# Optimization experiments

Hardware: AMD Instinct MI355X
Metric: run time of the kernel (lower is better)

## Reference

```python
import jax, jax.numpy as jnp
import numpy as np
import math

EMBED_DIM = 1024
NUM_HEADS = 16
HEAD_DIM = EMBED_DIM // NUM_HEADS
B, S = 4, 2048


def setup_inputs() -> dict:
    key = jax.random.key(0)
    ks = jax.random.split(key, 9)
    scale = 1.0 / math.sqrt(EMBED_DIM)
    def lin(k):
        kw, kb = jax.random.split(k)
        W = jax.random.uniform(kw, (EMBED_DIM, EMBED_DIM), jnp.float32, -scale, scale)
        b = jax.random.uniform(kb, (EMBED_DIM,), jnp.float32, -scale, scale)
        return W, b
    Wq, bq = lin(ks[0]); Wk, bk = lin(ks[1]); Wv, bv = lin(ks[2]); Wo, bo = lin(ks[3])
    x = jax.random.normal(ks[4], (B, S, EMBED_DIM), jnp.float32)
    return {"x": x, "Wq": Wq, "bq": bq, "Wk": Wk, "bk": bk,
            "Wv": Wv, "bv": bv, "Wo": Wo, "bo": bo}


def reference(x, Wq, bq, Wk, bk, Wv, bv, Wo, bo):
    Bx, Sx, E = x.shape
    def proj(W, b):
        y = jnp.einsum('bse,oe->bso', x, W) + b
        return y.reshape(Bx, Sx, NUM_HEADS, HEAD_DIM).transpose(0, 2, 1, 3)  # [B,H,S,D]
    q = proj(Wq, bq)
    k = proj(Wk, bk)
    v = proj(Wv, bv)
    scores = jnp.einsum('bhsd,bhtd->bhst', q, k) / math.sqrt(HEAD_DIM)
    # causal mask (paged_cache is None, seq_len > 1)
    causal = jnp.tril(jnp.ones((Sx, Sx), dtype=bool))
    scores = jnp.where(causal[None, None], scores, -jnp.inf)
    attn = jax.nn.softmax(scores, axis=-1)
    out = jnp.einsum('bhst,bhtd->bhsd', attn, v)
    out = out.transpose(0, 2, 1, 3).reshape(Bx, Sx, E)
    return jnp.einsum('bse,oe->bso', out, Wo) + bo
```

## Files before the change

### kernel.cpp

```cpp
#include <hip/hip_runtime.h>
#include <hip/hip_bf16.h>
#include <stdint.h>

#define EDIM 1024
#define NH   16
#define HD   64
#define BB   4
#define SS   2048
#define MROWS (BB*SS)

typedef __bf16 bf16x8 __attribute__((ext_vector_type(8)));
typedef __bf16 bf16x4 __attribute__((ext_vector_type(4)));
typedef float  f32x4  __attribute__((ext_vector_type(4)));
typedef float  f32x16 __attribute__((ext_vector_type(16)));
typedef int    int2v  __attribute__((ext_vector_type(2)));

__device__ __forceinline__ void async16(const void* g, void* lds) {
    __builtin_amdgcn_global_load_lds((__attribute__((address_space(1))) void*)(g),
                                     (__attribute__((address_space(3))) void*)(lds),
                                     16, 0, 0);
}

__device__ __forceinline__ f32x4 mfma16(bf16x8 a, bf16x8 b, f32x4 c) {
    return __builtin_amdgcn_mfma_f32_16x16x32_bf16(a, b, c, 0, 0, 0);
}
__device__ __forceinline__ f32x16 mfma32(bf16x8 a, bf16x8 b, f32x16 c) {
    return __builtin_amdgcn_mfma_f32_32x32x16_bf16(a, b, c, 0, 0, 0);
}

__device__ __forceinline__ int pkbf16(float a, float b) {
    union { __bf16 h[2]; int i; } u;
    u.h[0] = (__bf16)a; u.h[1] = (__bf16)b;
    return u.i;
}

__global__ __launch_bounds__(256) void cvt_kernel(const float* __restrict__ s,
                                                  __bf16* __restrict__ d, int n) {
    int i = (blockIdx.x * 256 + threadIdx.x) * 4;
    if (i < n) {
        float4 v = *reinterpret_cast<const float4*>(s + i);
        bf16x4 o;
        o.x = (__bf16)v.x; o.y = (__bf16)v.y; o.z = (__bf16)v.z; o.w = (__bf16)v.w;
        *reinterpret_cast<bf16x4*>(d + i) = o;
    }
}

__global__ __launch_bounds__(256) void cvt4_kernel(const float* __restrict__ s0,
                                                   const float* __restrict__ s1,
                                                   const float* __restrict__ s2,
                                                   const float* __restrict__ s3,
                                                   __bf16* __restrict__ d) {
    int m = blockIdx.x >> 10;
    const float* s = (m == 0) ? s0 : (m == 1) ? s1 : (m == 2) ? s2 : s3;
    int i = ((blockIdx.x & 1023) * 256 + threadIdx.x) * 4;
    float4 v = *reinterpret_cast<const float4*>(s + i);
    bf16x4 o;
    o.x = (__bf16)v.x; o.y = (__bf16)v.y; o.z = (__bf16)v.z; o.w = (__bf16)v.w;
    *reinterpret_cast<bf16x4*>(d + (size_t)m * (EDIM * EDIM) + i) = o;
}

struct GemmCtx {
    const __bf16 *ap0, *ap1, *bp0, *bp1;
    int wb0, wb1;
};

__device__ __forceinline__ void g_stage(GemmCtx& c, char* As, char* Bs) {
    async16(c.ap0, As + c.wb0);
    async16(c.ap1, As + c.wb1);
    async16(c.bp0, Bs + c.wb0);
    async16(c.bp1, Bs + c.wb1);
    c.ap0 += 32; c.ap1 += 32; c.bp0 += 32; c.bp1 += 32;
}

__device__ __forceinline__ void g_compute(const char* As, const char* Bs,
                                          int wm, int wn, int lrow, int lslot,
                                          f32x4 acc[4][4]) {
    bf16x8 af[4], bfr[4];
    #pragma unroll
    for (int mf = 0; mf < 4; ++mf) {
        int row = wm + mf * 16 + lrow;
        af[mf] = *reinterpret_cast<const bf16x8*>(As + row * 64 + ((lslot ^ (row & 3)) << 4));
    }
    #pragma unroll
    for (int nf = 0; nf < 4; ++nf) {
        int row = wn + nf * 16 + lrow;
        bfr[nf] = *reinterpret_cast<const bf16x8*>(Bs + row * 64 + ((lslot ^ (row & 3)) << 4));
    }
    __builtin_amdgcn_s_setprio(1);
    #pragma unroll
    for (int mf = 0; mf < 4; ++mf)
        #pragma unroll
        for (int nf = 0; nf < 4; ++nf)
            acc[mf][nf] = mfma16(af[mf], bfr[nf], acc[mf][nf]);
    __builtin_amdgcn_s_setprio(0);
}

#define GEMM_DBUF_LOOP()                                                      \
    g_stage(ctx, As0, Bs0);                                                   \
    for (int kt = 0; kt < 32; kt += 2) {                                      \
        g_stage(ctx, As1, Bs1);                                               \
        asm volatile("s_waitcnt vmcnt(4)" ::: "memory");                      \
        __builtin_amdgcn_s_barrier();                                         \
        __builtin_amdgcn_sched_barrier(0);                                    \
        g_compute(As0, Bs0, wm, wn, lrow, lslot, acc);                        \
        __builtin_amdgcn_sched_barrier(0);                                    \
        __builtin_amdgcn_s_barrier();                                         \
        if (kt + 2 < 32) {                                                    \
            g_stage(ctx, As0, Bs0);                                           \
            asm volatile("s_waitcnt vmcnt(4)" ::: "memory");                  \
        } else {                                                              \
            asm volatile("s_waitcnt vmcnt(0)" ::: "memory");                  \
        }                                                                     \
        __builtin_amdgcn_s_barrier();                                         \
        __builtin_amdgcn_sched_barrier(0);                                    \
        g_compute(As1, Bs1, wm, wn, lrow, lslot, acc);                        \
        __builtin_amdgcn_sched_barrier(0);                                    \
        __builtin_amdgcn_s_barrier();                                         \
    }

#define GEMM_PREAMBLE(Aptr, Wptr)                                             \
    const int tid = threadIdx.x;                                              \
    const int w = tid >> 6, l = tid & 63;                                     \
    const int bm = blockIdx.x * 128, bn = blockIdx.y * 128;                   \
    const int wm = (w >> 1) * 64, wn = (w & 1) * 64;                          \
    f32x4 acc[4][4] = {};                                                     \
    const int lrow = l & 15;                                                  \
    const int lslot = l >> 4;                                                 \
    const int row0 = tid >> 2, cb0 = tid & 3;                                 \
    const int row1 = 64 + row0;                                               \
    GemmCtx ctx;                                                              \
    ctx.ap0 = (Aptr) + (size_t)(bm + row0) * EDIM + ((cb0 ^ (row0 & 3)) << 3);\
    ctx.ap1 = (Aptr) + (size_t)(bm + row1) * EDIM + ((cb0 ^ (row1 & 3)) << 3);\
    ctx.bp0 = (Wptr) + (size_t)(bn + row0) * EDIM + ((cb0 ^ (row0 & 3)) << 3);\
    ctx.bp1 = (Wptr) + (size_t)(bn + row1) * EDIM + ((cb0 ^ (row1 & 3)) << 3);\
    ctx.wb0 = (w * 64) * 16;                                                  \
    ctx.wb1 = (256 + w * 64) * 16;

__global__ __launch_bounds__(256) void gemm_qkv(const __bf16* __restrict__ A,
                                                const __bf16* __restrict__ W,
                                                const float* __restrict__ bq,
                                                const float* __restrict__ bk,
                                                const float* __restrict__ bv,
                                                __bf16* __restrict__ Qb,
                                                __bf16* __restrict__ Kb,
                                                __bf16* __restrict__ Vtb) {
    __shared__ char As0[128 * 64], Bs0[128 * 64];
    __shared__ char As1[128 * 64], Bs1[128 * 64];
    GEMM_PREAMBLE(A, W)
    GEMM_DBUF_LOOP()

    const int mat = bn >> 10;
    const float* bias = (mat == 0) ? bq : (mat == 1) ? bk : bv;
    __bf16* qk = (mat == 0) ? Qb : Kb;

    #pragma unroll
    for (int nf = 0; nf < 4; ++nf) {
        int ng = bn + wn + nf * 16 + lrow;
        int nn = ng & 1023;
        int h = nn >> 6, d = nn & 63;
        float bval = bias[nn];
        #pragma unroll
        for (int mf = 0; mf < 4; ++mf) {
            #pragma unroll
            for (int r = 0; r < 4; ++r) {
                int mg = bm + wm + mf * 16 + (l >> 4) * 4 + r;
                float v = acc[mf][nf][r] + bval;
                int b = mg >> 11, s = mg & 2047;
                if (mat == 2)
                    Vtb[((size_t)(b * NH + h) * HD + d) * SS + s] = (__bf16)v;
                else
                    qk[((size_t)(b * NH + h) * SS + s) * HD + d] = (__bf16)v;
            }
        }
    }
}

__global__ __launch_bounds__(256) void gemm_out(const __bf16* __restrict__ A,
                                                const __bf16* __restrict__ W,
                                                const float* __restrict__ bias,
                                                float* __restrict__ dst) {
    __shared__ char As0[128 * 64], Bs0[128 * 64];
    __shared__ char As1[128 * 64], Bs1[128 * 64];
    GEMM_PREAMBLE(A, W)
    GEMM_DBUF_LOOP()

    #pragma unroll
    for (int nf = 0; nf < 4; ++nf) {
        int ng = bn + wn + nf * 16 + lrow;
        float bval = bias[ng];
        #pragma unroll
        for (int mf = 0; mf < 4; ++mf) {
            #pragma unroll
            for (int r = 0; r < 4; ++r) {
                int mg = bm + wm + mf * 16 + (l >> 4) * 4 + r;
                dst[(size_t)mg * EDIM + ng] = acc[mf][nf][r] + bval;
            }
        }
    }
}

#define SCL2E 0.18033688f

__global__ __launch_bounds__(512) void attn_kernel(const __bf16* __restrict__ Q,
                                                   const __bf16* __restrict__ K,
                                                   const __bf16* __restrict__ Vt,
                                                   __bf16* __restrict__ Oa) {
    __shared__ char ks0[64 * 128], vs0[64 * 128];
    __shared__ char ks1[64 * 128], vs1[64 * 128];

    const int bh = blockIdx.x;
    const int qt = 7 - blockIdx.y;
    const int tid = threadIdx.x;
    const int w = tid >> 6;
    const int l = tid & 63;
    const int lo = l & 31;
    const int hi = l >> 5;

    const __bf16* Qp = Q + (size_t)bh * (SS * HD);
    const __bf16* Kp = K + (size_t)bh * (SS * HD);
    const __bf16* Vp = Vt + (size_t)bh * (HD * SS);

    const int qg = qt * 256 + w * 32 + lo;
    bf16x8 qf[4];
    #pragma unroll
    for (int kc = 0; kc < 4; ++kc)
        qf[kc] = *reinterpret_cast<const bf16x8*>(Qp + (size_t)qg * HD + kc * 16 + hi * 8);

    const int rowS = tid >> 3, cbS = tid & 7;
    const int gsS = (cbS ^ (rowS & 7)) << 3;
    const int wb = w * 1024;
    const __bf16* kp = Kp + (size_t)rowS * HD + gsS;
    const __bf16* vp = Vp + (size_t)rowS * SS + gsS;

    f32x16 oacc[2] = {};
    float mrow = -1e30f;
    float lsum = 0.f;

    const int qwhi = qt * 256 + w * 32 + 31;
    const int ntiles = 4 * qt + 4;

    auto compute = [&](const char* ksb, const char* vsb, int kv0) {
        f32x16 acc[2] = {};
        __builtin_amdgcn_s_setprio(1);
        #pragma unroll
        for (int tb = 0; tb < 2; ++tb) {
            const int t = tb * 32 + lo;
            const char* krow = ksb + t * 128;
            const int tx = (t & 7);
            #pragma unroll
            for (int kc = 0; kc < 4; ++kc) {
                bf16x8 kf = *reinterpret_cast<const bf16x8*>(krow + ((2 * kc + hi) ^ tx) * 16);
                acc[tb] = mfma32(kf, qf[kc], acc[tb]);
            }
        }
        __builtin_amdgcn_s_setprio(0);

        if (kv0 + 63 > qg - lo) {
            #pragma unroll
            for (int tb = 0; tb < 2; ++tb)
                #pragma unroll
                for (int r = 0; r < 16; ++r) {
                    int t = kv0 + tb * 32 + ((r & 3) + 8 * (r >> 2)) + 4 * hi;
                    if (t > qg) acc[tb][r] = -1e30f;
                }
        }

        float mx = acc[0][0];
        #pragma unroll
        for (int r = 1; r < 16; ++r) mx = fmaxf(mx, acc[0][r]);
        #pragma unroll
        for (int r = 0; r < 16; ++r) mx = fmaxf(mx, acc[1][r]);
        mx = fmaxf(mx, __shfl_xor(mx, 32));
        float mxs = mx * SCL2E;
        if (!__all(mxs <= mrow + 8.0f)) {
            float mnew = fmaxf(mrow, mxs);
            float alpha = exp2f(mrow - mnew);
            mrow = mnew;
            lsum *= alpha;
            oacc[0] *= alpha;
            oacc[1] *= alpha;
        }
        float psum = 0.f;
        #pragma unroll
        for (int tb = 0; tb < 2; ++tb)
            #pragma unroll
            for (int r = 0; r < 16; ++r) {
                float p = exp2f(fmaf(acc[tb][r], SCL2E, -mrow));
                acc[tb][r] = p;
                psum += p;
            }
        lsum += psum;

        bf16x8 pa[4];
        #pragma unroll
        for (int ks2 = 0; ks2 < 4; ++ks2) {
            const int tb = ks2 >> 1, rb = (ks2 & 1) * 8;
            int a0 = pkbf16(acc[tb][rb + 0], acc[tb][rb + 1]);
            int b0 = pkbf16(acc[tb][rb + 4], acc[tb][rb + 5]);
            int a1 = pkbf16(acc[tb][rb + 2], acc[tb][rb + 3]);
            int b1 = pkbf16(acc[tb][rb + 6], acc[tb][rb + 7]);
            int2v s1 = __builtin_amdgcn_permlane32_swap(a0, b0, false, false);
            int2v s2 = __builtin_amdgcn_permlane32_swap(a1, b1, false, false);
            union { int i[4]; bf16x8 v; } u;
            u.i[0] = s1[0]; u.i[1] = s2[0]; u.i[2] = s1[1]; u.i[3] = s2[1];
            pa[ks2] = u.v;
        }

        __builtin_amdgcn_s_setprio(1);
        #pragma unroll
        for (int ks2 = 0; ks2 < 4; ++ks2) {
            #pragma unroll
            for (int db = 0; db < 2; ++db) {
                const int d = db * 32 + lo;
                bf16x8 vb = *reinterpret_cast<const bf16x8*>(
                    vsb + d * 128 + (((2 * ks2 + hi) ^ (d & 7)) * 16));
                oacc[db] = mfma32(vb, pa[ks2], oacc[db]);
            }
        }
        __builtin_amdgcn_s_setprio(0);
    };

    async16(kp, ks0 + wb);
    async16(vp, vs0 + wb);
    kp += 64 * HD; vp += 64;

    for (int kt = 0; kt < ntiles; kt += 2) {
        async16(kp, ks1 + wb);
        async16(vp, vs1 + wb);
        kp += 64 * HD; vp += 64;
        asm volatile("s_waitcnt vmcnt(2)" ::: "memory");
        __builtin_amdgcn_s_barrier();
        __builtin_amdgcn_sched_barrier(0);
        if (kt * 64 <= qwhi) compute(ks0, vs0, kt * 64);
        __builtin_amdgcn_sched_barrier(0);
        __builtin_amdgcn_s_barrier();

        if (kt + 2 < ntiles) {
            async16(kp, ks0 + wb);
            async16(vp, vs0 + wb);
            kp += 64 * HD; vp += 64;
            asm volatile("s_waitcnt vmcnt(2)" ::: "memory");
        } else {
            asm volatile("s_waitcnt vmcnt(0)" ::: "memory");
        }
        __builtin_amdgcn_s_barrier();
        __builtin_amdgcn_sched_barrier(0);
        if ((kt + 1) * 64 <= qwhi) compute(ks1, vs1, (kt + 1) * 64);
        __builtin_amdgcn_sched_barrier(0);
        __builtin_amdgcn_s_barrier();
    }

    const int b = bh >> 4, h = bh & 15;
    float lsumt = lsum + __shfl_xor(lsum, 32);
    float inv = 1.0f / lsumt;
    __bf16* orow = Oa + ((size_t)(b * SS + qg)) * EDIM + h * HD;
    #pragma unroll
    for (int db = 0; db < 2; ++db) {
        #pragma unroll
        for (int g = 0; g < 4; ++g) {
            int d0 = db * 32 + g * 8 + 4 * hi;
            bf16x4 o4;
            o4.x = (__bf16)(oacc[db][g * 4 + 0] * inv);
            o4.y = (__bf16)(oacc[db][g * 4 + 1] * inv);
            o4.z = (__bf16)(oacc[db][g * 4 + 2] * inv);
            o4.w = (__bf16)(oacc[db][g * 4 + 3] * inv);
            *reinterpret_cast<bf16x4*>(orow + d0) = o4;
        }
    }
}

extern "C" void kernel_launch(void* const* d_in, const int* in_sizes, int n_in,
                              void* d_out, int out_size, void* d_ws, size_t ws_size,
                              hipStream_t stream) {
    const float* x  = (const float*)d_in[0];
    const float* Wq = (const float*)d_in[1];
    const float* bq = (const float*)d_in[2];
    const float* Wk = (const float*)d_in[3];
    const float* bk = (const float*)d_in[4];
    const float* Wv = (const float*)d_in[5];
    const float* bv = (const float*)d_in[6];
    const float* Wo = (const float*)d_in[7];
    const float* bo = (const float*)d_in[8];

    char* ws = (char*)d_ws;
    const size_t SZ_XB  = (size_t)MROWS * EDIM * 2;
    const size_t SZ_W   = (size_t)EDIM * EDIM * 2;
    const size_t SZ_QKV = (size_t)BB * NH * SS * HD * 2;

    __bf16* xb  = (__bf16*)(ws);
    __bf16* wqb = (__bf16*)(ws + SZ_XB);
    __bf16* wob = (__bf16*)(ws + SZ_XB + 3 * SZ_W);
    __bf16* Qb  = (__bf16*)(ws + SZ_XB + 4 * SZ_W);
    __bf16* Kb  = (__bf16*)(ws + SZ_XB + 4 * SZ_W + SZ_QKV);
    __bf16* Vtb = (__bf16*)(ws + SZ_XB + 4 * SZ_W + 2 * SZ_QKV);
    __bf16* Oab = (__bf16*)(ws + SZ_XB + 4 * SZ_W + 3 * SZ_QKV);

    cvt_kernel<<<MROWS * EDIM / 1024, 256, 0, stream>>>(x, xb, MROWS * EDIM);
    cvt4_kernel<<<4096, 256, 0, stream>>>(Wq, Wk, Wv, Wo, wqb);

    gemm_qkv<<<dim3(MROWS / 128, 3 * EDIM / 128), 256, 0, stream>>>(
        xb, wqb, bq, bk, bv, Qb, Kb, Vtb);

    attn_kernel<<<dim3(BB * NH, 8), 512, 0, stream>>>(Qb, Kb, Vtb, Oab);

    gemm_out<<<dim3(MROWS / 128, EDIM / 128), 256, 0, stream>>>(
        Oab, wob, bo, (float*)d_out);
}
```

Before: 203.2 us.

## Split KV range of long causal query tiles across two blocks and merge

The four longest causal query tiles (qt 4..7) are each split into two blocks that handle halves of the KV range, writing unnormalized bf16 partial outputs plus (max, sum) stats to workspace. A new merge kernel combines the halves with log-sum-exp rescaling and writes the normalized output. This balances the causal triangle's work across more blocks (768 instead of 512) to reduce tail imbalance, at the cost of an extra kernel launch, extra partial-output traffic, and bf16 rounding of unnormalized partials. The workspace regions reused for the partials (xb and the start of the weights area) are assumed dead by then, but wob lies just after and must not be overlapped.

```diff
diff --git a/kernel.cpp b/kernel.cpp
--- a/kernel.cpp
+++ b/kernel.cpp
@@ -204,12 +204,17 @@
 __global__ __launch_bounds__(512) void attn_kernel(const __bf16* __restrict__ Q,
                                                    const __bf16* __restrict__ K,
                                                    const __bf16* __restrict__ Vt,
-                                                   __bf16* __restrict__ Oa) {
+                                                   __bf16* __restrict__ Oa,
+                                                   __bf16* __restrict__ Opart,
+                                                   float2* __restrict__ Ml) {
     __shared__ char ks0[64 * 128], vs0[64 * 128];
     __shared__ char ks1[64 * 128], vs1[64 * 128];
 
     const int bh = blockIdx.x;
-    const int qt = 7 - blockIdx.y;
+    const int y = blockIdx.y;
+    const bool split = (y < 8);
+    const int qt = split ? (7 - (y >> 1)) : (11 - y);
+    const int half = split ? (y & 1) : 0;
     const int tid = threadIdx.x;
     const int w = tid >> 6;
     const int l = tid & 63;
@@ -226,18 +231,21 @@
     for (int kc = 0; kc < 4; ++kc)
         qf[kc] = *reinterpret_cast<const bf16x8*>(Qp + (size_t)qg * HD + kc * 16 + hi * 8);
 
+    const int nt_all = 4 * qt + 4;
+    const int tcount = split ? (nt_all >> 1) : nt_all;
+    const int kt0 = split ? (half * tcount) : 0;
+
     const int rowS = tid >> 3, cbS = tid & 7;
     const int gsS = (cbS ^ (rowS & 7)) << 3;
     const int wb = w * 1024;
-    const __bf16* kp = Kp + (size_t)rowS * HD + gsS;
-    const __bf16* vp = Vp + (size_t)rowS * SS + gsS;
+    const __bf16* kp = Kp + (size_t)(kt0 * 64 + rowS) * HD + gsS;
+    const __bf16* vp = Vp + (size_t)rowS * SS + kt0 * 64 + gsS;
 
     f32x16 oacc[2] = {};
     float mrow = -1e30f;
     float lsum = 0.f;
 
     const int qwhi = qt * 256 + w * 32 + 31;
-    const int ntiles = 4 * qt + 4;
 
     auto compute = [&](const char* ksb, const char* vsb, int kv0) {
         f32x16 acc[2] = {};
@@ -324,18 +332,18 @@
     async16(vp, vs0 + wb);
     kp += 64 * HD; vp += 64;
 
-    for (int kt = 0; kt < ntiles; kt += 2) {
+    for (int kt = 0; kt < tcount; kt += 2) {
         async16(kp, ks1 + wb);
         async16(vp, vs1 + wb);
         kp += 64 * HD; vp += 64;
         asm volatile("s_waitcnt vmcnt(2)" ::: "memory");
         __builtin_amdgcn_s_barrier();
         __builtin_amdgcn_sched_barrier(0);
-        if (kt * 64 <= qwhi) compute(ks0, vs0, kt * 64);
+        if ((kt0 + kt) * 64 <= qwhi) compute(ks0, vs0, (kt0 + kt) * 64);
         __builtin_amdgcn_sched_barrier(0);
         __builtin_amdgcn_s_barrier();
 
-        if (kt + 2 < ntiles) {
+        if (kt + 2 < tcount) {
             async16(kp, ks0 + wb);
             async16(vp, vs0 + wb);
             kp += 64 * HD; vp += 64;
@@ -345,28 +353,71 @@
         }
         __builtin_amdgcn_s_barrier();
         __builtin_amdgcn_sched_barrier(0);
-        if ((kt + 1) * 64 <= qwhi) compute(ks1, vs1, (kt + 1) * 64);
+        if ((kt0 + kt + 1) * 64 <= qwhi) compute(ks1, vs1, (kt0 + kt + 1) * 64);
         __builtin_amdgcn_sched_barrier(0);
         __builtin_amdgcn_s_barrier();
     }
 
-    const int b = bh >> 4, h = bh & 15;
     float lsumt = lsum + __shfl_xor(lsum, 32);
-    float inv = 1.0f / lsumt;
-    __bf16* orow = Oa + ((size_t)(b * SS + qg)) * EDIM + h * HD;
-    #pragma unroll
-    for (int db = 0; db < 2; ++db) {
-        #pragma unroll
-        for (int g = 0; g < 4; ++g) {
-            int d0 = db * 32 + g * 8 + 4 * hi;
-            bf16x4 o4;
-            o4.x = (__bf16)(oacc[db][g * 4 + 0] * inv);
-            o4.y = (__bf16)(oacc[db][g * 4 + 1] * inv);
-            o4.z = (__bf16)(oacc[db][g * 4 + 2] * inv);
-            o4.w = (__bf16)(oacc[db][g * 4 + 3] * inv);
-            *reinterpret_cast<bf16x4*>(orow + d0) = o4;
-        }
-    }
+    if (split) {
+        const int qp = qg - 1024;
+        __bf16* prow = Opart + (((size_t)(half * 64 + bh) * 1024) + qp) * 64;
+        #pragma unroll
+        for (int db = 0; db < 2; ++db) {
+            #pragma unroll
+            for (int g = 0; g < 4; ++g) {
+                int d0 = db * 32 + g * 8 + 4 * hi;
+                bf16x4 o4;
+                o4.x = (__bf16)oacc[db][g * 4 + 0];
+                o4.y = (__bf16)oacc[db][g * 4 + 1];
+                o4.z = (__bf16)oacc[db][g * 4 + 2];
+                o4.w = (__bf16)oacc[db][g * 4 + 3];
+                *reinterpret_cast<bf16x4*>(prow + d0) = o4;
+            }
+        }
+        if (hi == 0)
+            Ml[(size_t)(half * 64 + bh) * 1024 + qp] = make_float2(mrow, lsumt);
+    } else {
+        const int b = bh >> 4, h = bh & 15;
+        float inv = 1.0f / lsumt;
+        __bf16* orow = Oa + ((size_t)(b * SS + qg)) * EDIM + h * HD;
+        #pragma unroll
+        for (int db = 0; db < 2; ++db) {
+            #pragma unroll
+            for (int g = 0; g < 4; ++g) {
+                int d0 = db * 32 + g * 8 + 4 * hi;
+                bf16x4 o4;
+                o4.x = (__bf16)(oacc[db][g * 4 + 0] * inv);
+                o4.y = (__bf16)(oacc[db][g * 4 + 1] * inv);
+                o4.z = (__bf16)(oacc[db][g * 4 + 2] * inv);
+                o4.w = (__bf16)(oacc[db][g * 4 + 3] * inv);
+                *reinterpret_cast<bf16x4*>(orow + d0) = o4;
+            }
+        }
+    }
+}
+
+__global__ __launch_bounds__(256) void merge_kernel(const __bf16* __restrict__ Opart,
+                                                    const float2* __restrict__ Ml,
+                                                    __bf16* __restrict__ Oa) {
+    int t = blockIdx.x * 256 + threadIdx.x;
+    int d8 = t & 7;
+    int qp = (t >> 3) & 1023;
+    int bh = t >> 13;
+    size_t r0 = ((size_t)bh * 1024 + qp);
+    size_t r1 = ((size_t)(64 + bh) * 1024 + qp);
+    float2 ml0 = Ml[r0], ml1 = Ml[r1];
+    float m = fmaxf(ml0.x, ml1.x);
+    float a0 = exp2f(ml0.x - m), a1 = exp2f(ml1.x - m);
+    float inv = 1.0f / (a0 * ml0.y + a1 * ml1.y);
+    bf16x8 o0 = *reinterpret_cast<const bf16x8*>(Opart + r0 * 64 + d8 * 8);
+    bf16x8 o1 = *reinterpret_cast<const bf16x8*>(Opart + r1 * 64 + d8 * 8);
+    bf16x8 r;
+    #pragma unroll
+    for (int j = 0; j < 8; ++j)
+        r[j] = (__bf16)((a0 * (float)o0[j] + a1 * (float)o1[j]) * inv);
+    int b = bh >> 4, h = bh & 15, q = 1024 + qp;
+    *reinterpret_cast<bf16x8*>(Oa + ((size_t)(b * SS + q)) * EDIM + h * HD + d8 * 8) = r;
 }
 
 extern "C" void kernel_launch(void* const* d_in, const int* in_sizes, int n_in,
@@ -394,6 +445,8 @@
     __bf16* Kb  = (__bf16*)(ws + SZ_XB + 4 * SZ_W + SZ_QKV);
     __bf16* Vtb = (__bf16*)(ws + SZ_XB + 4 * SZ_W + 2 * SZ_QKV);
     __bf16* Oab = (__bf16*)(ws + SZ_XB + 4 * SZ_W + 3 * SZ_QKV);
+    __bf16* Opart = (__bf16*)(ws);
+    float2* Mlb   = (float2*)(ws + SZ_XB);
 
     cvt_kernel<<<MROWS * EDIM / 1024, 256, 0, stream>>>(x, xb, MROWS * EDIM);
     cvt4_kernel<<<4096, 256, 0, stream>>>(Wq, Wk, Wv, Wo, wqb);
@@ -401,7 +454,8 @@
     gemm_qkv<<<dim3(MROWS / 128, 3 * EDIM / 128), 256, 0, stream>>>(
         xb, wqb, bq, bk, bv, Qb, Kb, Vtb);
 
-    attn_kernel<<<dim3(BB * NH, 8), 512, 0, stream>>>(Qb, Kb, Vtb, Oab);
+    attn_kernel<<<dim3(BB * NH, 12), 512, 0, stream>>>(Qb, Kb, Vtb, Oab, Opart, Mlb);
+    merge_kernel<<<64 * 1024 * 8 / 256, 256, 0, stream>>>(Opart, Mlb, Oab);
 
     gemm_out<<<dim3(MROWS / 128, EDIM / 128), 256, 0, stream>>>(
         Oab, wob, bo, (float*)d_out);
```

Result: no change. 201.6 us (-0.8%).
